# Performance work log

Hardware: AMD Instinct MI355X
Metric: run time of the kernel (lower is better)

Reference implementation:

```python
import jax, jax.numpy as jnp
import numpy as np
from jax import lax

B, S, D, STEPS, OUT = 512, 256, 256, 256, 3


def setup_inputs() -> dict:
    key = jax.random.key(0)
    ks = jax.random.split(key, 16)
    sc = 0.05
    n = lambda k, shp: jax.random.normal(k, shp, jnp.float32) * sc
    return {
        "e_all": jax.random.normal(ks[0], (B, S, D), jnp.float32),
        "e_last": jax.random.normal(ks[1], (1, B, D), jnp.float32),
        # NN_Attention params
        "Wa": n(ks[2], (D, D)), "ba": n(ks[3], (D,)),
        "Ua": n(ks[4], (D, D)), "bu": n(ks[5], (D,)),
        "Va": n(ks[6], (D,)), "bv": n(ks[7], ()),
        # GRU params (PyTorch layout: W_ih [3D, 3+D], W_hh [3D, D])
        "W_ih": n(ks[8], (3 * D, D + 3)), "b_ih": n(ks[9], (3 * D,)),
        "W_hh": n(ks[10], (3 * D, D)), "b_hh": n(ks[11], (3 * D,)),
        # output linear D -> 3
        "Wo": n(ks[12], (OUT, D)), "bo": n(ks[13], (OUT,)),
    }


def _decode(e_all, e_last, Wa, ba, Ua, bu, Va, bv, W_ih, b_ih, W_hh, b_hh, Wo, bo):
    # Ua(keys) is constant across steps -> precompute once (same math)
    Ua_keys = jnp.einsum('bsd,ed->bse', e_all, Ua) + bu  # [B, S, D]

    def step(carry, _):
        h, x_in = carry
        # Bahdanau attention: Va(tanh(Wa(q) + Ua(keys)))
        q = h @ Wa.T + ba                                       # [B, D]
        scores = jnp.einsum('bsd,d->bs', jnp.tanh(q[:, None, :] + Ua_keys), Va) + bv
        w = jax.nn.softmax(scores, axis=-1)                     # [B, S]
        ctx = jnp.einsum('bs,bsd->bd', w, e_all)                # [B, D]
        # GRU cell on input [context ; d_input] (cat order matches torch code)
        x = jnp.concatenate([ctx, x_in], axis=-1)               # [B, D+3]
        gi = x @ W_ih.T + b_ih
        gh = h @ W_hh.T + b_hh
        i_r, i_z, i_n = jnp.split(gi, 3, axis=-1)
        h_r, h_z, h_n = jnp.split(gh, 3, axis=-1)
        r = jax.nn.sigmoid(i_r + h_r)
        z = jax.nn.sigmoid(i_z + h_z)
        nn_ = jnp.tanh(i_n + r * h_n)
        h_new = (1.0 - z) * nn_ + z * h
        out = h_new @ Wo.T + bo                                 # [B, 3]
        return (h_new, out), (out, w)

    h0 = e_last[0]                                              # [B, D]
    x0 = jnp.zeros((h0.shape[0], OUT), h0.dtype)
    (hT, _), (outs, ws) = lax.scan(step, (h0, x0), None, length=STEPS)
    d_outputs = outs.transpose(1, 0, 2)                         # [B, STEPS, 3]
    cross_attn = ws.transpose(1, 0, 2).reshape(h0.shape[0], 1, STEPS * S)
    return d_outputs, hT[None], cross_attn


def reference(e_all, e_last, Wa, ba, Ua, bu, Va, bv, W_ih, b_ih, W_hh, b_hh, Wo, bo):
    return _decode(e_all, e_last, Wa, ba, Ua, bu, Va, bv, W_ih, b_ih, W_hh, b_hh, Wo, bo)
```

## Files before the change

### kernel.cpp

```cpp
#include <hip/hip_runtime.h>
#include <hip/hip_bf16.h>
#include <stdint.h>

#define NB 512
#define NS 256
#define ND 256
#define NT 256
#define NO 3

#define LOG2E 1.44269504088896340736f
#define C2 (2.0f*LOG2E)

#if __has_builtin(__builtin_amdgcn_exp2f)
__device__ __forceinline__ float exp2_fast(float x){ return __builtin_amdgcn_exp2f(x); }
#else
__device__ __forceinline__ float exp2_fast(float x){ return exp2f(x); }
#endif
#if __has_builtin(__builtin_amdgcn_rcpf)
__device__ __forceinline__ float rcp_fast(float x){ return __builtin_amdgcn_rcpf(x); }
#else
__device__ __forceinline__ float rcp_fast(float x){ return 1.0f/x; }
#endif

__device__ __forceinline__ float tanh_f(float x){
  float e = exp2_fast(x * C2);
  return 1.0f - 2.0f*rcp_fast(e + 1.0f);
}
__device__ __forceinline__ float sigm_f(float x){
  return rcp_fast(1.0f + exp2_fast(-x*LOG2E));
}
__device__ __forceinline__ float bflo(uint32_t u){ return __uint_as_float(u<<16); }
__device__ __forceinline__ float bfhi(uint32_t u){ return __uint_as_float(u & 0xffff0000u); }
__device__ __forceinline__ uint16_t f2bf(float f){
  uint32_t u = __float_as_uint(f);
  return (uint16_t)((u + 0x7fffu + ((u>>16)&1u)) >> 16);
}
__device__ __forceinline__ uint32_t pack2(float a, float b){
  return (uint32_t)f2bf(a) | ((uint32_t)f2bf(b) << 16);
}

#if __has_builtin(__builtin_amdgcn_fdot2_f32_bf16)
typedef __bf16 bfp2 __attribute__((ext_vector_type(2)));
__device__ __forceinline__ float dot2bf(uint32_t a, uint32_t b, float c){
  return __builtin_amdgcn_fdot2_f32_bf16(__builtin_bit_cast(bfp2, a),
                                         __builtin_bit_cast(bfp2, b), c, false);
}
#else
__device__ __forceinline__ float dot2bf(uint32_t a, uint32_t b, float c){
  return c + bflo(a)*bflo(b) + bfhi(a)*bfhi(b);
}
#endif


__global__ void k_transpose(const float* __restrict__ src, float* __restrict__ dst,
                            int R, int C){
  int idx = blockIdx.x*256 + threadIdx.x;
  if (idx < R*C){
    int r = idx / C, c = idx - r*C;
    dst[c*R + r] = src[idx];
  }
}

__global__ void __launch_bounds__(256) k_uk(const float* __restrict__ e_all,
    const float* __restrict__ UaT, const float* __restrict__ bu,
    uint16_t* __restrict__ UK){
  __shared__ float At[ND][20];
  const int t = threadIdx.x;
  const int m0 = blockIdx.x * 16;
  const int b  = m0 >> 8;
  const int s0 = m0 & (NS-1);
  #pragma unroll
  for (int i=0;i<16;i++)
    At[t][i] = e_all[(size_t)(m0+i)*ND + t];
  __syncthreads();
  float acc[16];
  float bue = bu[t];
  #pragma unroll
  for (int i=0;i<16;i++) acc[i] = bue;
  for (int d=0; d<ND; ++d){
    float u = UaT[d*ND + t];
    const float4 a0 = *(const float4*)&At[d][0];
    const float4 a1 = *(const float4*)&At[d][4];
    const float4 a2 = *(const float4*)&At[d][8];
    const float4 a3 = *(const float4*)&At[d][12];
    acc[0]+=a0.x*u;  acc[1]+=a0.y*u;  acc[2]+=a0.z*u;  acc[3]+=a0.w*u;
    acc[4]+=a1.x*u;  acc[5]+=a1.y*u;  acc[6]+=a1.z*u;  acc[7]+=a1.w*u;
    acc[8]+=a2.x*u;  acc[9]+=a2.y*u;  acc[10]+=a2.z*u; acc[11]+=a2.w*u;
    acc[12]+=a3.x*u; acc[13]+=a3.y*u; acc[14]+=a3.z*u; acc[15]+=a3.w*u;
  }
  const int e8 = t>>3, j = t&7;
  uint16_t* base = UK + (size_t)b*NS*ND + (size_t)e8*(NS*8) + j;
  #pragma unroll
  for (int i=0;i<16;i++)
    base[(size_t)(s0+i)*8] = f2bf(acc[i] * C2);
}

__global__ void k_ep(const float* __restrict__ e_all, uint32_t* __restrict__ EP){
  int idx = blockIdx.x*256 + threadIdx.x;
  if (idx >= NB*128*256) return;
  int d  = idx & 255;
  int s2 = (idx >> 8) & 127;
  int b  = idx >> 15;
  float e0 = e_all[((size_t)b*NS + 2*s2  )*ND + d];
  float e1 = e_all[((size_t)b*NS + 2*s2+1)*ND + d];
  EP[idx] = pack2(e0, e1);
}

__global__ void k_pkq(const float* __restrict__ W_ih, const float* __restrict__ W_hh,
                      uint32_t* __restrict__ PKq){
  int idx = blockIdx.x*256 + threadIdx.x;
  if (idx >= 260*3*256) return;
  int d  = idx & 255;
  int gk = idx >> 8;
  int k2 = gk/3, g = gk - 3*k2;
  int col = g*256 + d;
  float w0 = 0.f, w1 = 0.f;
  if (k2 < 130){
    int k0 = 2*k2, k1 = k0+1;
    w0 = W_ih[(size_t)col*259 + k0];
    w1 = (k1 < 259) ? W_ih[(size_t)col*259 + k1] : 0.f;
  } else if (k2 < 258){
    int kk = 2*(k2-130);
    w0 = W_hh[(size_t)col*256 + kk];
    w1 = W_hh[(size_t)col*256 + kk+1];
  }
  PKq[idx] = pack2(w0, w1);
}

__global__ void k_pack_q(const float* __restrict__ Wa, uint32_t* __restrict__ PQ){
  int idx = blockIdx.x*256 + threadIdx.x;
  if (idx >= 128*256) return;
  int d = idx & 255, k2 = idx >> 8;
  PQ[idx] = pack2(Wa[(size_t)d*256 + 2*k2], Wa[(size_t)d*256 + 2*k2 + 1]);
}

__global__ void __launch_bounds__(1024, 4) k_decode(
    const uint16_t* __restrict__ UK, const uint32_t* __restrict__ EP,
    const uint32_t* __restrict__ PKq, const uint32_t* __restrict__ PQ,
    const float* __restrict__ e_last,
    const float* __restrict__ Va, const float* __restrict__ bv,
    const float* __restrict__ b_ih, const float* __restrict__ b_hh,
    const float* __restrict__ ba, const float* __restrict__ bo,
    const float* __restrict__ Wo,
    float* __restrict__ dout, float* __restrict__ hT_out, float* __restrict__ ca)
{
  __shared__ float    hf[2][ND];
  __shared__ float    xin[2][4];
  __shared__ uint32_t xb[2][260];
  __shared__ __align__(16) float qL[2][ND];
  __shared__ __align__(16) float va2[ND];
  __shared__ float    WoL[3*ND];
  __shared__ float    qpart[2][2][ND];
  __shared__ float    spart[2][2][ND];
  __shared__ __align__(16) float cpart[2][8][ND];
  __shared__ float    gpart[2][4][3][ND];
  __shared__ uint32_t wb[2][128];
  __shared__ float    red[16];

  const int t    = threadIdx.x;
  const int d    = t & 255;
  const int q4   = t >> 8;
  const int bi   = q4 >> 1;
  const int half = q4 & 1;
  const int lane = t & 63;
  const int w    = t >> 6;
  const int b0   = blockIdx.x * 2;

  if (q4 == 0){
    hf[0][d] = e_last[(size_t)b0*ND + d];
    va2[d]   = 2.0f*Va[d];
    WoL[d] = Wo[d]; WoL[256+d] = Wo[256+d]; WoL[512+d] = Wo[512+d];
    if (d < 4){ xin[0][d]=0.f; xin[1][d]=0.f; }
  } else if (q4 == 1){
    hf[1][d] = e_last[(size_t)(b0+1)*ND + d];
  }
  const float bias_r  = b_ih[d]     + b_hh[d];
  const float bias_z  = b_ih[256+d] + b_hh[256+d];
  const float bias_ni = b_ih[512+d];
  const float bias_nh = b_hh[512+d];
  const float ba_d = ba[d];
  const float bv0  = bv[0];
  const float bo0 = bo[0], bo1 = bo[1], bo2 = bo[2];
  __syncthreads();
  if (t < 256){
    int bb = t>>7, i = t&127;
    xb[bb][130+i] = pack2(hf[bb][2*i], hf[bb][2*i+1]);
  }
  if (t == 256){
    xb[0][128]=0u; xb[0][129]=0u; xb[0][258]=0u; xb[0][259]=0u;
    xb[1][128]=0u; xb[1][129]=0u; xb[1][258]=0u; xb[1][259]=0u;
  }
  float sumVaH = 0.f;
  {
    #pragma unroll 8
    for (int e = half*128; e < half*128+128; ++e) sumVaH += va2[e];
    sumVaH *= 0.5f;
  }
  __syncthreads();

  const uint16_t* ukb  = UK + (size_t)(b0+bi)*NS*ND + (size_t)half*16*2048 + (size_t)d*8;
  const uint32_t* epbw = EP + (size_t)(b0+(w>>3))*128*256;
  float* ca_bq = ca + (size_t)(b0 + (q4&1))*(NT*NS);

  #pragma unroll 1
  for (int step=0; step<NT; ++step){
    {
      float aq = 0.f;
      const uint32_t* pq = PQ + (size_t)(half*64)*256 + d;
      const uint32_t* xh = &xb[bi][130 + half*64];
      #pragma unroll 1
      for (int kk=0; kk<64; kk+=8){
        uint32_t wv[8], xv[8];
        #pragma unroll
        for (int j=0;j<8;j++){ wv[j] = pq[(kk+j)*256]; xv[j] = xh[kk+j]; }
        #pragma unroll
        for (int j=0;j<8;j++) aq = dot2bf(wv[j], xv[j], aq);
      }
      qpart[bi][half][d] = aq;
    }
    __syncthreads();
    if (q4 < 2)
      qL[q4][d] = (qpart[q4][0][d] + qpart[q4][1][d] + ba_d) * C2;
    __syncthreads();

    {
      float acc = 0.f;
      #pragma unroll 1
      for (int g=0; g<16; g+=8){
        uint4 u[8];
        #pragma unroll
        for (int j=0;j<8;j++) u[j] = *(const uint4*)(ukb + (size_t)(g+j)*2048);
        #pragma unroll
        for (int j=0;j<8;j++){
          const int e0 = half*128 + (g+j)*8;
          const float4 q0 = *(const float4*)&qL[bi][e0];
          const float4 q1 = *(const float4*)&qL[bi][e0+4];
          const float4 v0 = *(const float4*)&va2[e0];
          const float4 v1 = *(const float4*)&va2[e0+4];
          float r;
          r = rcp_fast(exp2_fast(bflo(u[j].x)+q0.x)+1.f); acc = fmaf(v0.x, r, acc);
          r = rcp_fast(exp2_fast(bfhi(u[j].x)+q0.y)+1.f); acc = fmaf(v0.y, r, acc);
          r = rcp_fast(exp2_fast(bflo(u[j].y)+q0.z)+1.f); acc = fmaf(v0.z, r, acc);
          r = rcp_fast(exp2_fast(bfhi(u[j].y)+q0.w)+1.f); acc = fmaf(v0.w, r, acc);
          r = rcp_fast(exp2_fast(bflo(u[j].z)+q1.x)+1.f); acc = fmaf(v1.x, r, acc);
          r = rcp_fast(exp2_fast(bfhi(u[j].z)+q1.y)+1.f); acc = fmaf(v1.y, r, acc);
          r = rcp_fast(exp2_fast(bflo(u[j].w)+q1.z)+1.f); acc = fmaf(v1.z, r, acc);
          r = rcp_fast(exp2_fast(bfhi(u[j].w)+q1.w)+1.f); acc = fmaf(v1.w, r, acc);
        }
      }
      spart[bi][half][d] = sumVaH - acc;
    }
    __syncthreads();

    float p_reg = 0.f;
    if (q4 < 2){
      float sc = spart[q4][0][d] + spart[q4][1][d] + bv0;
      p_reg = exp2_fast(sc * LOG2E);
      float ssum = p_reg;
      #pragma unroll
      for (int o=32;o;o>>=1) ssum += __shfl_xor(ssum, o);
      if (lane==0) red[w] = ssum;
    }
    __syncthreads();
    if (q4 < 2){
      const int rb = q4*4;
      float ssum = (red[rb]+red[rb+1]) + (red[rb+2]+red[rb+3]);
      float wgt = p_reg * rcp_fast(ssum);
      __builtin_nontemporal_store(wgt, &ca_bq[(size_t)step*NS + d]);
      float other = __shfl_xor(wgt, 1);
      if (!(d&1)) wb[q4][d>>1] = pack2(wgt, other);
    }
    __syncthreads();

    {
      const int cb = w>>3, sub = w&7;
      float c0=0,c1=0,c2=0,c3=0;
      const int s0 = sub*16;
      #pragma unroll 1
      for (int g=0; g<16; g+=8){
        uint4 ev[8]; uint32_t wp[8];
        #pragma unroll
        for (int j=0;j<8;j++){
          ev[j] = *(const uint4*)(epbw + (size_t)(s0+g+j)*256 + lane*4);
          wp[j] = wb[cb][s0+g+j];
        }
        #pragma unroll
        for (int j=0;j<8;j++){
          c0 = dot2bf(ev[j].x, wp[j], c0);
          c1 = dot2bf(ev[j].y, wp[j], c1);
          c2 = dot2bf(ev[j].z, wp[j], c2);
          c3 = dot2bf(ev[j].w, wp[j], c3);
        }
      }
      *(float4*)&cpart[cb][sub][lane*4] = make_float4(c0,c1,c2,c3);
    }
    __syncthreads();
    if (q4 < 2){
      float cx = 0.f;
      #pragma unroll
      for (int i=0;i<8;i++) cx += cpart[q4][i][d];
      float other = __shfl_xor(cx, 1);
      if (!(d&1)) xb[q4][d>>1] = pack2(cx, other);
      if (d==128) xb[q4][128] = pack2(xin[q4][0], xin[q4][1]);
      if (d==129) xb[q4][129] = pack2(xin[q4][2], 0.f);
    }
    __syncthreads();

    {
      float a0r=0,a0z=0,a0n=0, a1r=0,a1z=0,a1n=0;
      const int k0 = q4*65;
      const uint32_t* pk = PKq + (size_t)k0*768 + d;
      #pragma unroll 1
      for (int g=0; g<64; g+=8){
        uint32_t wr[8], wz[8], wn[8], x0[8], x1[8];
        #pragma unroll
        for (int j=0;j<8;j++){
          const uint32_t* p = pk + (size_t)(g+j)*768;
          wr[j]=p[0]; wz[j]=p[256]; wn[j]=p[512];
          x0[j]=xb[0][k0+g+j]; x1[j]=xb[1][k0+g+j];
        }
        #pragma unroll
        for (int j=0;j<8;j++){
          a0r=dot2bf(wr[j],x0[j],a0r); a0z=dot2bf(wz[j],x0[j],a0z); a0n=dot2bf(wn[j],x0[j],a0n);
          a1r=dot2bf(wr[j],x1[j],a1r); a1z=dot2bf(wz[j],x1[j],a1z); a1n=dot2bf(wn[j],x1[j],a1n);
        }
      }
      {
        const uint32_t* p = pk + (size_t)64*768;
        uint32_t w0=p[0], w1=p[256], w2=p[512];
        uint32_t xa=xb[0][k0+64], xc=xb[1][k0+64];
        a0r=dot2bf(w0,xa,a0r); a0z=dot2bf(w1,xa,a0z); a0n=dot2bf(w2,xa,a0n);
        a1r=dot2bf(w0,xc,a1r); a1z=dot2bf(w1,xc,a1z); a1n=dot2bf(w2,xc,a1n);
      }
      gpart[0][q4][0][d]=a0r; gpart[0][q4][1][d]=a0z; gpart[0][q4][2][d]=a0n;
      gpart[1][q4][0][d]=a1r; gpart[1][q4][1][d]=a1z; gpart[1][q4][2][d]=a1n;
    }
    __syncthreads();
    if (q4 < 2){
      float ar  = (gpart[q4][0][0][d]+gpart[q4][1][0][d]) + (gpart[q4][2][0][d]+gpart[q4][3][0][d]) + bias_r;
      float az  = (gpart[q4][0][1][d]+gpart[q4][1][1][d]) + (gpart[q4][2][1][d]+gpart[q4][3][1][d]) + bias_z;
      float ani =  gpart[q4][0][2][d]+gpart[q4][1][2][d] + bias_ni;
      float anh =  gpart[q4][2][2][d]+gpart[q4][3][2][d] + bias_nh;
      float rg = sigm_f(ar);
      float zg = sigm_f(az);
      float ng = tanh_f(ani + rg*anh);
      float hnew = (1.f-zg)*ng + zg*hf[q4][d];
      hf[q4][d] = hnew;
      float other = __shfl_xor(hnew, 1);
      if (!(d&1)) xb[q4][130 + (d>>1)] = pack2(hnew, other);
    }
    __syncthreads();

    if ((w & 7) == 0){
      const int bq = w >> 3;
      float p0=0,p1=0,p2=0;
      #pragma unroll
      for (int i=0;i<4;i++){
        float hv = hf[bq][i*64 + lane];
        p0 = fmaf(hv, WoL[      i*64+lane], p0);
        p1 = fmaf(hv, WoL[256 + i*64+lane], p1);
        p2 = fmaf(hv, WoL[512 + i*64+lane], p2);
      }
      #pragma unroll
      for (int o=32;o;o>>=1){
        p0+=__shfl_xor(p0,o); p1+=__shfl_xor(p1,o); p2+=__shfl_xor(p2,o);
      }
      if (lane==0){
        float o0=p0+bo0, o1=p1+bo1, o2=p2+bo2;
        float* do_b = dout + (size_t)(b0+bq)*(NT*NO);
        __builtin_nontemporal_store(o0, &do_b[(size_t)step*NO+0]);
        __builtin_nontemporal_store(o1, &do_b[(size_t)step*NO+1]);
        __builtin_nontemporal_store(o2, &do_b[(size_t)step*NO+2]);
        xin[bq][0]=o0; xin[bq][1]=o1; xin[bq][2]=o2;
      }
    }
  }

  __syncthreads();
  if (q4 < 2) hT_out[(size_t)(b0+q4)*ND + d] = hf[q4][d];
}


extern "C" void kernel_launch(void* const* d_in, const int* in_sizes, int n_in,
                              void* d_out, int out_size, void* d_ws, size_t ws_size,
                              hipStream_t stream) {
  const float* e_all  = (const float*)d_in[0];
  const float* e_last = (const float*)d_in[1];
  const float* Wa     = (const float*)d_in[2];
  const float* ba     = (const float*)d_in[3];
  const float* Ua     = (const float*)d_in[4];
  const float* bu     = (const float*)d_in[5];
  const float* Va     = (const float*)d_in[6];
  const float* bv     = (const float*)d_in[7];
  const float* W_ih   = (const float*)d_in[8];
  const float* b_ih   = (const float*)d_in[9];
  const float* W_hh   = (const float*)d_in[10];
  const float* b_hh   = (const float*)d_in[11];
  const float* Wo     = (const float*)d_in[12];
  const float* bo     = (const float*)d_in[13];

  char* ws = (char*)d_ws;
  uint16_t* UK   = (uint16_t*)(ws + 0ull);
  uint32_t* EP   = (uint32_t*)(ws + 67108864ull);
  float*    UaT  = (float*)(ws + 134217728ull);
  uint32_t* PKq  = (uint32_t*)(ws + 134217728ull);
  uint32_t* PQ   = (uint32_t*)(ws + 135016448ull);

  float* dout = (float*)d_out;
  float* hT   = dout + (size_t)NB*NT*NO;
  float* ca   = hT   + (size_t)NB*ND;

  k_transpose<<<(ND*ND+255)/256,256,0,stream>>>(Ua, UaT, ND, ND);
  k_uk<<<NB*NS/16,256,0,stream>>>(e_all, UaT, bu, UK);
  k_ep<<<(NB*128*256+255)/256,256,0,stream>>>(e_all, EP);
  k_pkq<<<(260*3*256+255)/256,256,0,stream>>>(W_ih, W_hh, PKq);
  k_pack_q<<<(128*256+255)/256,256,0,stream>>>(Wa, PQ);

  k_decode<<<NB/2,1024,0,stream>>>(UK, EP, PKq, PQ, e_last, Va, bv,
                                   b_ih, b_hh, ba, bo, Wo, dout, hT, ca);
}
```

Baseline: 7.738 ms.

## Use MFMA bf16 for query projection and GRU gate matmuls per step

Replaces the per-step dot2 bf16 loops for the Wa query projection and the GRU input/hidden gate products with 16x16x32 bf16 MFMA instructions. A 16-row LDS panel holds the two batch rows (context, previous output, hidden) padded to 16, and each wave computes 16 output columns. Weights are repacked row-major in bf16 for MFMA B operands, and the partial-sum LDS buffers and their extra syncs are removed. The cost is that 14 of the 16 MFMA rows are wasted padding, and B operands are read from global memory each step.

Measured after the change: 15.08 ms. 1.95x slower.

```diff
diff --git a/kernel.cpp b/kernel.cpp
--- a/kernel.cpp
+++ b/kernel.cpp
@@ -7,9 +7,14 @@
 #define ND 256
 #define NT 256
 #define NO 3
+#define KG 544
+#define PROW 552
 
 #define LOG2E 1.44269504088896340736f
 #define C2 (2.0f*LOG2E)
+
+typedef short short8v __attribute__((ext_vector_type(8)));
+typedef float f32x4   __attribute__((ext_vector_type(4)));
 
 #if __has_builtin(__builtin_amdgcn_exp2f)
 __device__ __forceinline__ float exp2_fast(float x){ return __builtin_amdgcn_exp2f(x); }
@@ -50,6 +55,10 @@
   return c + bflo(a)*bflo(b) + bfhi(a)*bfhi(b);
 }
 #endif
+
+__device__ __forceinline__ f32x4 mfma_bf16(short8v a, short8v b, f32x4 c){
+  return __builtin_amdgcn_mfma_f32_16x16x32_bf16(a, b, c, 0, 0, 0);
+}
 
 
 __global__ void k_transpose(const float* __restrict__ src, float* __restrict__ dst,
@@ -106,37 +115,26 @@
   EP[idx] = pack2(e0, e1);
 }
 
-__global__ void k_pkq(const float* __restrict__ W_ih, const float* __restrict__ W_hh,
-                      uint32_t* __restrict__ PKq){
+__global__ void k_wg(const float* __restrict__ W_ih, const float* __restrict__ W_hh,
+                     uint16_t* __restrict__ Wg){
   int idx = blockIdx.x*256 + threadIdx.x;
-  if (idx >= 260*3*256) return;
-  int d  = idx & 255;
-  int gk = idx >> 8;
-  int k2 = gk/3, g = gk - 3*k2;
-  int col = g*256 + d;
-  float w0 = 0.f, w1 = 0.f;
-  if (k2 < 130){
-    int k0 = 2*k2, k1 = k0+1;
-    w0 = W_ih[(size_t)col*259 + k0];
-    w1 = (k1 < 259) ? W_ih[(size_t)col*259 + k1] : 0.f;
-  } else if (k2 < 258){
-    int kk = 2*(k2-130);
-    w0 = W_hh[(size_t)col*256 + kk];
-    w1 = W_hh[(size_t)col*256 + kk+1];
-  }
-  PKq[idx] = pack2(w0, w1);
-}
-
-__global__ void k_pack_q(const float* __restrict__ Wa, uint32_t* __restrict__ PQ){
+  if (idx >= 768*KG) return;
+  int n = idx / KG, k = idx - n*KG;
+  float v = 0.f;
+  if (k < 259)       v = W_ih[(size_t)n*259 + k];
+  else if (k >= 288) v = W_hh[(size_t)n*256 + (k-288)];
+  Wg[idx] = f2bf(v);
+}
+
+__global__ void k_wq(const float* __restrict__ Wa, uint16_t* __restrict__ Wq){
   int idx = blockIdx.x*256 + threadIdx.x;
-  if (idx >= 128*256) return;
-  int d = idx & 255, k2 = idx >> 8;
-  PQ[idx] = pack2(Wa[(size_t)d*256 + 2*k2], Wa[(size_t)d*256 + 2*k2 + 1]);
+  if (idx >= ND*ND) return;
+  Wq[idx] = f2bf(Wa[idx]);
 }
 
 __global__ void __launch_bounds__(1024, 4) k_decode(
     const uint16_t* __restrict__ UK, const uint32_t* __restrict__ EP,
-    const uint32_t* __restrict__ PKq, const uint32_t* __restrict__ PQ,
+    const uint16_t* __restrict__ Wg, const uint16_t* __restrict__ Wq,
     const float* __restrict__ e_last,
     const float* __restrict__ Va, const float* __restrict__ bv,
     const float* __restrict__ b_ih, const float* __restrict__ b_hh,
@@ -144,16 +142,14 @@
     const float* __restrict__ Wo,
     float* __restrict__ dout, float* __restrict__ hT_out, float* __restrict__ ca)
 {
+  __shared__ __align__(16) uint16_t panelA[16*PROW];
   __shared__ float    hf[2][ND];
   __shared__ float    xin[2][4];
-  __shared__ uint32_t xb[2][260];
   __shared__ __align__(16) float qL[2][ND];
   __shared__ __align__(16) float va2[ND];
   __shared__ float    WoL[3*ND];
-  __shared__ float    qpart[2][2][ND];
   __shared__ float    spart[2][2][ND];
   __shared__ __align__(16) float cpart[2][8][ND];
-  __shared__ float    gpart[2][4][3][ND];
   __shared__ uint32_t wb[2][128];
   __shared__ float    red[16];
 
@@ -166,30 +162,23 @@
   const int w    = t >> 6;
   const int b0   = blockIdx.x * 2;
 
+  for (int i=t; i<16*PROW; i+=1024) panelA[i] = 0;
   if (q4 == 0){
-    hf[0][d] = e_last[(size_t)b0*ND + d];
-    va2[d]   = 2.0f*Va[d];
+    va2[d] = 2.0f*Va[d];
     WoL[d] = Wo[d]; WoL[256+d] = Wo[256+d]; WoL[512+d] = Wo[512+d];
     if (d < 4){ xin[0][d]=0.f; xin[1][d]=0.f; }
-  } else if (q4 == 1){
-    hf[1][d] = e_last[(size_t)(b0+1)*ND + d];
-  }
-  const float bias_r  = b_ih[d]     + b_hh[d];
-  const float bias_z  = b_ih[256+d] + b_hh[256+d];
-  const float bias_ni = b_ih[512+d];
-  const float bias_nh = b_hh[512+d];
-  const float ba_d = ba[d];
-  const float bv0  = bv[0];
+  }
+  if (q4 < 2) hf[q4][d] = e_last[(size_t)(b0+q4)*ND + d];
+  const int ncol = (w<<4) + (lane & 15);
+  const float biasR  = b_ih[ncol]     + b_hh[ncol];
+  const float biasZ  = b_ih[256+ncol] + b_hh[256+ncol];
+  const float biasNi = b_ih[512+ncol];
+  const float biasNh = b_hh[512+ncol];
+  const float baq    = ba[ncol];
+  const float bv0 = bv[0];
   const float bo0 = bo[0], bo1 = bo[1], bo2 = bo[2];
   __syncthreads();
-  if (t < 256){
-    int bb = t>>7, i = t&127;
-    xb[bb][130+i] = pack2(hf[bb][2*i], hf[bb][2*i+1]);
-  }
-  if (t == 256){
-    xb[0][128]=0u; xb[0][129]=0u; xb[0][258]=0u; xb[0][259]=0u;
-    xb[1][128]=0u; xb[1][129]=0u; xb[1][258]=0u; xb[1][259]=0u;
-  }
+  if (q4 < 2) panelA[q4*PROW + 288 + d] = f2bf(hf[q4][d]);
   float sumVaH = 0.f;
   {
     #pragma unroll 8
@@ -202,25 +191,28 @@
   const uint32_t* epbw = EP + (size_t)(b0+(w>>3))*128*256;
   float* ca_bq = ca + (size_t)(b0 + (q4&1))*(NT*NS);
 
+  const uint16_t* apG = panelA + (lane&15)*PROW + ((lane>>4)*8);
+  const uint16_t* apQ = apG + 288;
+  const uint16_t* bQ  = Wq + (size_t)(ncol)*ND + ((lane>>4)*8);
+  const uint16_t* bR  = Wg + (size_t)(ncol)*KG + ((lane>>4)*8);
+  const uint16_t* bZ  = bR + (size_t)256*KG;
+  const uint16_t* bN  = bR + (size_t)512*KG;
+
   #pragma unroll 1
   for (int step=0; step<NT; ++step){
     {
-      float aq = 0.f;
-      const uint32_t* pq = PQ + (size_t)(half*64)*256 + d;
-      const uint32_t* xh = &xb[bi][130 + half*64];
-      #pragma unroll 1
-      for (int kk=0; kk<64; kk+=8){
-        uint32_t wv[8], xv[8];
-        #pragma unroll
-        for (int j=0;j<8;j++){ wv[j] = pq[(kk+j)*256]; xv[j] = xh[kk+j]; }
-        #pragma unroll
-        for (int j=0;j<8;j++) aq = dot2bf(wv[j], xv[j], aq);
-      }
-      qpart[bi][half][d] = aq;
-    }
-    __syncthreads();
-    if (q4 < 2)
-      qL[q4][d] = (qpart[q4][0][d] + qpart[q4][1][d] + ba_d) * C2;
+      f32x4 aq = {0.f,0.f,0.f,0.f};
+      #pragma unroll
+      for (int ks=0; ks<8; ++ks){
+        short8v av = *(const short8v*)(apQ + ks*32);
+        short8v bvv= *(const short8v*)(bQ  + ks*32);
+        aq = mfma_bf16(av, bvv, aq);
+      }
+      if (lane < 16){
+        qL[0][ncol] = (aq[0] + baq) * C2;
+        qL[1][ncol] = (aq[1] + baq) * C2;
+      }
+    }
     __syncthreads();
 
     {
@@ -299,55 +291,40 @@
       float cx = 0.f;
       #pragma unroll
       for (int i=0;i<8;i++) cx += cpart[q4][i][d];
-      float other = __shfl_xor(cx, 1);
-      if (!(d&1)) xb[q4][d>>1] = pack2(cx, other);
-      if (d==128) xb[q4][128] = pack2(xin[q4][0], xin[q4][1]);
-      if (d==129) xb[q4][129] = pack2(xin[q4][2], 0.f);
+      panelA[q4*PROW + d] = f2bf(cx);
+      if (d < 3) panelA[q4*PROW + 256 + d] = f2bf(xin[q4][d]);
     }
     __syncthreads();
 
     {
-      float a0r=0,a0z=0,a0n=0, a1r=0,a1z=0,a1n=0;
-      const int k0 = q4*65;
-      const uint32_t* pk = PKq + (size_t)k0*768 + d;
-      #pragma unroll 1
-      for (int g=0; g<64; g+=8){
-        uint32_t wr[8], wz[8], wn[8], x0[8], x1[8];
-        #pragma unroll
-        for (int j=0;j<8;j++){
-          const uint32_t* p = pk + (size_t)(g+j)*768;
-          wr[j]=p[0]; wz[j]=p[256]; wn[j]=p[512];
-          x0[j]=xb[0][k0+g+j]; x1[j]=xb[1][k0+g+j];
+      f32x4 aR = {0,0,0,0}, aZ = {0,0,0,0}, aNi = {0,0,0,0}, aNh = {0,0,0,0};
+      #pragma unroll
+      for (int ks=0; ks<9; ++ks){
+        short8v av = *(const short8v*)(apG + ks*32);
+        aR  = mfma_bf16(av, *(const short8v*)(bR + ks*32), aR);
+        aZ  = mfma_bf16(av, *(const short8v*)(bZ + ks*32), aZ);
+        aNi = mfma_bf16(av, *(const short8v*)(bN + ks*32), aNi);
+      }
+      #pragma unroll
+      for (int ks=9; ks<17; ++ks){
+        short8v av = *(const short8v*)(apG + ks*32);
+        aR  = mfma_bf16(av, *(const short8v*)(bR + ks*32), aR);
+        aZ  = mfma_bf16(av, *(const short8v*)(bZ + ks*32), aZ);
+        aNh = mfma_bf16(av, *(const short8v*)(bN + ks*32), aNh);
+      }
+      __syncthreads();
+      if (lane < 16){
+        #pragma unroll
+        for (int m=0; m<2; ++m){
+          float rg = sigm_f(aR[m] + biasR);
+          float zg = sigm_f(aZ[m] + biasZ);
+          float ng = tanh_f((aNi[m] + biasNi) + rg*(aNh[m] + biasNh));
+          float hold = hf[m][ncol];
+          float hnew = (1.f - zg)*ng + zg*hold;
+          hf[m][ncol] = hnew;
+          panelA[m*PROW + 288 + ncol] = f2bf(hnew);
         }
-        #pragma unroll
-        for (int j=0;j<8;j++){
-          a0r=dot2bf(wr[j],x0[j],a0r); a0z=dot2bf(wz[j],x0[j],a0z); a0n=dot2bf(wn[j],x0[j],a0n);
-          a1r=dot2bf(wr[j],x1[j],a1r); a1z=dot2bf(wz[j],x1[j],a1z); a1n=dot2bf(wn[j],x1[j],a1n);
-        }
-      }
-      {
-        const uint32_t* p = pk + (size_t)64*768;
-        uint32_t w0=p[0], w1=p[256], w2=p[512];
-        uint32_t xa=xb[0][k0+64], xc=xb[1][k0+64];
-        a0r=dot2bf(w0,xa,a0r); a0z=dot2bf(w1,xa,a0z); a0n=dot2bf(w2,xa,a0n);
-        a1r=dot2bf(w0,xc,a1r); a1z=dot2bf(w1,xc,a1z); a1n=dot2bf(w2,xc,a1n);
-      }
-      gpart[0][q4][0][d]=a0r; gpart[0][q4][1][d]=a0z; gpart[0][q4][2][d]=a0n;
-      gpart[1][q4][0][d]=a1r; gpart[1][q4][1][d]=a1z; gpart[1][q4][2][d]=a1n;
-    }
-    __syncthreads();
-    if (q4 < 2){
-      float ar  = (gpart[q4][0][0][d]+gpart[q4][1][0][d]) + (gpart[q4][2][0][d]+gpart[q4][3][0][d]) + bias_r;
-      float az  = (gpart[q4][0][1][d]+gpart[q4][1][1][d]) + (gpart[q4][2][1][d]+gpart[q4][3][1][d]) + bias_z;
-      float ani =  gpart[q4][0][2][d]+gpart[q4][1][2][d] + bias_ni;
-      float anh =  gpart[q4][2][2][d]+gpart[q4][3][2][d] + bias_nh;
-      float rg = sigm_f(ar);
-      float zg = sigm_f(az);
-      float ng = tanh_f(ani + rg*anh);
-      float hnew = (1.f-zg)*ng + zg*hf[q4][d];
-      hf[q4][d] = hnew;
-      float other = __shfl_xor(hnew, 1);
-      if (!(d&1)) xb[q4][130 + (d>>1)] = pack2(hnew, other);
+      }
     }
     __syncthreads();
 
@@ -400,11 +377,11 @@
   const float* bo     = (const float*)d_in[13];
 
   char* ws = (char*)d_ws;
-  uint16_t* UK   = (uint16_t*)(ws + 0ull);
-  uint32_t* EP   = (uint32_t*)(ws + 67108864ull);
-  float*    UaT  = (float*)(ws + 134217728ull);
-  uint32_t* PKq  = (uint32_t*)(ws + 134217728ull);
-  uint32_t* PQ   = (uint32_t*)(ws + 135016448ull);
+  uint16_t* UK  = (uint16_t*)(ws + 0ull);
+  uint32_t* EP  = (uint32_t*)(ws + 67108864ull);
+  uint16_t* Wg  = (uint16_t*)(ws + 134217728ull);
+  uint16_t* Wq  = (uint16_t*)(ws + 135053312ull);
+  float*    UaT = (float*)   (ws + 135184384ull);
 
   float* dout = (float*)d_out;
   float* hT   = dout + (size_t)NB*NT*NO;
@@ -413,9 +390,9 @@
   k_transpose<<<(ND*ND+255)/256,256,0,stream>>>(Ua, UaT, ND, ND);
   k_uk<<<NB*NS/16,256,0,stream>>>(e_all, UaT, bu, UK);
   k_ep<<<(NB*128*256+255)/256,256,0,stream>>>(e_all, EP);
-  k_pkq<<<(260*3*256+255)/256,256,0,stream>>>(W_ih, W_hh, PKq);
-  k_pack_q<<<(128*256+255)/256,256,0,stream>>>(Wa, PQ);
-
-  k_decode<<<NB/2,1024,0,stream>>>(UK, EP, PKq, PQ, e_last, Va, bv,
+  k_wg<<<(768*KG+255)/256,256,0,stream>>>(W_ih, W_hh, Wg);
+  k_wq<<<(ND*ND+255)/256,256,0,stream>>>(Wa, Wq);
+
+  k_decode<<<NB/2,1024,0,stream>>>(UK, EP, Wg, Wq, e_last, Va, bv,
                                    b_ih, b_hh, ba, bo, Wo, dout, hT, ca);
 }
```

## Store precomputed keys and encoder states as FP8 E4M3 instead of bf16

Applied to the files above, without the earlier changes.

The precomputed Ua(keys) tensor and the packed encoder states are now quantized to FP8 E4M3, with custom encode kernels, new interleaved layouts and hardware fp8-to-f32 packed conversion in the decode loop. This halves the bytes the per-step attention and context loops stream from global memory or cache on every decode step. The cost is much coarser precision on activations (3-bit mantissa), which may exceed the accuracy tolerance, plus added conversion instructions in the hot loops.

After: 16.39 ms. 2.12x slower.

```diff
diff --git a/kernel.cpp b/kernel.cpp
--- a/kernel.cpp
+++ b/kernel.cpp
@@ -10,6 +10,8 @@
 
 #define LOG2E 1.44269504088896340736f
 #define C2 (2.0f*LOG2E)
+
+typedef float f32x2 __attribute__((ext_vector_type(2)));
 
 #if __has_builtin(__builtin_amdgcn_exp2f)
 __device__ __forceinline__ float exp2_fast(float x){ return __builtin_amdgcn_exp2f(x); }
@@ -51,6 +53,47 @@
 }
 #endif
 
+__device__ __forceinline__ uint8_t enc_e4m3(float x){
+  uint32_t sign = (__float_as_uint(x) >> 31) << 7;
+  float y = fminf(fabsf(x), 448.0f);
+  uint32_t u = __float_as_uint(y);
+  int e = (int)(u >> 23) - 127;
+  uint32_t code;
+  if (e < -6){
+    code = (uint32_t)__float2int_rn(y * 512.0f);
+  } else {
+    uint32_t r = u + 0x000FFFFFu + ((u >> 20) & 1u);
+    e = (int)(r >> 23) - 127;
+    code = (uint32_t)((e + 7) << 3) | ((r >> 20) & 7u);
+    if (code > 0x7Eu) code = 0x7Eu;
+  }
+  return (uint8_t)(sign | code);
+}
+
+#if __has_builtin(__builtin_amdgcn_cvt_pk_f32_fp8)
+template<bool HI>
+__device__ __forceinline__ f32x2 cvtpk_fp8(uint32_t w){
+  return __builtin_amdgcn_cvt_pk_f32_fp8((int)w, HI);
+}
+#else
+__device__ __forceinline__ float dec1_e4m3(uint32_t b){
+  uint32_t s = (b >> 7) << 31;
+  uint32_t em = b & 0x7fu;
+  float mag;
+  if (em >= 8u){
+    mag = __uint_as_float((((em >> 3) + 120u) << 23) | ((em & 7u) << 20));
+  } else {
+    mag = (float)em * 0.001953125f;
+  }
+  return __uint_as_float(s | __float_as_uint(mag));
+}
+template<bool HI>
+__device__ __forceinline__ f32x2 cvtpk_fp8(uint32_t w){
+  uint32_t p = HI ? (w >> 16) : (w & 0xffffu);
+  f32x2 r; r.x = dec1_e4m3(p & 0xffu); r.y = dec1_e4m3(p >> 8); return r;
+}
+#endif
+
 
 __global__ void k_transpose(const float* __restrict__ src, float* __restrict__ dst,
                             int R, int C){
@@ -63,7 +106,7 @@
 
 __global__ void __launch_bounds__(256) k_uk(const float* __restrict__ e_all,
     const float* __restrict__ UaT, const float* __restrict__ bu,
-    uint16_t* __restrict__ UK){
+    uint8_t* __restrict__ UKQ){
   __shared__ float At[ND][20];
   const int t = threadIdx.x;
   const int m0 = blockIdx.x * 16;
@@ -88,22 +131,29 @@
     acc[8]+=a2.x*u;  acc[9]+=a2.y*u;  acc[10]+=a2.z*u; acc[11]+=a2.w*u;
     acc[12]+=a3.x*u; acc[13]+=a3.y*u; acc[14]+=a3.z*u; acc[15]+=a3.w*u;
   }
-  const int e8 = t>>3, j = t&7;
-  uint16_t* base = UK + (size_t)b*NS*ND + (size_t)e8*(NS*8) + j;
+  const int e16 = t>>4, j = t&15;
+  uint8_t* base = UKQ + (((size_t)b*16 + e16)*256 + s0)*16 + j;
   #pragma unroll
-  for (int i=0;i<16;i++)
-    base[(size_t)(s0+i)*8] = f2bf(acc[i] * C2);
-}
-
-__global__ void k_ep(const float* __restrict__ e_all, uint32_t* __restrict__ EP){
+  for (int i=0;i<16;i++){
+    uint32_t mine = enc_e4m3(acc[i] * C2);
+    uint32_t other = (uint32_t)__shfl_xor((int)mine, 1);
+    if (!(t & 1))
+      *(uint16_t*)(base + (size_t)i*16) = (uint16_t)(mine | (other << 8));
+  }
+}
+
+__global__ void k_epq(const float* __restrict__ e_all, uint32_t* __restrict__ EPQ){
   int idx = blockIdx.x*256 + threadIdx.x;
-  if (idx >= NB*128*256) return;
+  if (idx >= NB*64*256) return;
   int d  = idx & 255;
-  int s2 = (idx >> 8) & 127;
-  int b  = idx >> 15;
-  float e0 = e_all[((size_t)b*NS + 2*s2  )*ND + d];
-  float e1 = e_all[((size_t)b*NS + 2*s2+1)*ND + d];
-  EP[idx] = pack2(e0, e1);
+  int s4 = (idx >> 8) & 63;
+  int b  = idx >> 14;
+  const float* e = e_all + ((size_t)b*NS + 4*s4)*ND + d;
+  uint32_t v = (uint32_t)enc_e4m3(e[0])
+             | ((uint32_t)enc_e4m3(e[ND])   << 8)
+             | ((uint32_t)enc_e4m3(e[2*ND]) << 16)
+             | ((uint32_t)enc_e4m3(e[3*ND]) << 24);
+  EPQ[idx] = v;
 }
 
 __global__ void k_pkq(const float* __restrict__ W_ih, const float* __restrict__ W_hh,
@@ -135,7 +185,7 @@
 }
 
 __global__ void __launch_bounds__(1024, 4) k_decode(
-    const uint16_t* __restrict__ UK, const uint32_t* __restrict__ EP,
+    const uint8_t* __restrict__ UKQ, const uint32_t* __restrict__ EPQ,
     const uint32_t* __restrict__ PKq, const uint32_t* __restrict__ PQ,
     const float* __restrict__ e_last,
     const float* __restrict__ Va, const float* __restrict__ bv,
@@ -154,7 +204,7 @@
   __shared__ float    spart[2][2][ND];
   __shared__ __align__(16) float cpart[2][8][ND];
   __shared__ float    gpart[2][4][3][ND];
-  __shared__ uint32_t wb[2][128];
+  __shared__ __align__(16) float wl[2][NS];
   __shared__ float    red[16];
 
   const int t    = threadIdx.x;
@@ -198,8 +248,8 @@
   }
   __syncthreads();
 
-  const uint16_t* ukb  = UK + (size_t)(b0+bi)*NS*ND + (size_t)half*16*2048 + (size_t)d*8;
-  const uint32_t* epbw = EP + (size_t)(b0+(w>>3))*128*256;
+  const uint8_t*  ukq  = UKQ + (((size_t)(b0+bi)*16 + half*8)*256 + d)*16;
+  const uint32_t* epqw = EPQ + (size_t)(b0+(w>>3))*64*256;
   float* ca_bq = ca + (size_t)(b0 + (q4&1))*(NT*NS);
 
   #pragma unroll 1
@@ -225,27 +275,25 @@
 
     {
       float acc = 0.f;
-      #pragma unroll 1
-      for (int g=0; g<16; g+=8){
-        uint4 u[8];
+      uint4 u[8];
+      #pragma unroll
+      for (int j=0;j<8;j++) u[j] = *(const uint4*)(ukq + (size_t)j*4096);
+      #pragma unroll
+      for (int j=0;j<8;j++){
+        const int e0g = half*128 + j*16;
         #pragma unroll
-        for (int j=0;j<8;j++) u[j] = *(const uint4*)(ukb + (size_t)(g+j)*2048);
-        #pragma unroll
-        for (int j=0;j<8;j++){
-          const int e0 = half*128 + (g+j)*8;
-          const float4 q0 = *(const float4*)&qL[bi][e0];
-          const float4 q1 = *(const float4*)&qL[bi][e0+4];
-          const float4 v0 = *(const float4*)&va2[e0];
-          const float4 v1 = *(const float4*)&va2[e0+4];
+        for (int dw=0; dw<4; ++dw){
+          const uint32_t dwv = (dw==0)?u[j].x:(dw==1)?u[j].y:(dw==2)?u[j].z:u[j].w;
+          const int eb = e0g + dw*4;
+          const f32x2 lo = cvtpk_fp8<false>(dwv);
+          const f32x2 hi = cvtpk_fp8<true>(dwv);
+          const float4 qq = *(const float4*)&qL[bi][eb];
+          const float4 vv = *(const float4*)&va2[eb];
           float r;
-          r = rcp_fast(exp2_fast(bflo(u[j].x)+q0.x)+1.f); acc = fmaf(v0.x, r, acc);
-          r = rcp_fast(exp2_fast(bfhi(u[j].x)+q0.y)+1.f); acc = fmaf(v0.y, r, acc);
-          r = rcp_fast(exp2_fast(bflo(u[j].y)+q0.z)+1.f); acc = fmaf(v0.z, r, acc);
-          r = rcp_fast(exp2_fast(bfhi(u[j].y)+q0.w)+1.f); acc = fmaf(v0.w, r, acc);
-          r = rcp_fast(exp2_fast(bflo(u[j].z)+q1.x)+1.f); acc = fmaf(v1.x, r, acc);
-          r = rcp_fast(exp2_fast(bfhi(u[j].z)+q1.y)+1.f); acc = fmaf(v1.y, r, acc);
-          r = rcp_fast(exp2_fast(bflo(u[j].w)+q1.z)+1.f); acc = fmaf(v1.z, r, acc);
-          r = rcp_fast(exp2_fast(bfhi(u[j].w)+q1.w)+1.f); acc = fmaf(v1.w, r, acc);
+          r = rcp_fast(exp2_fast(lo.x + qq.x) + 1.f); acc = fmaf(vv.x, r, acc);
+          r = rcp_fast(exp2_fast(lo.y + qq.y) + 1.f); acc = fmaf(vv.y, r, acc);
+          r = rcp_fast(exp2_fast(hi.x + qq.z) + 1.f); acc = fmaf(vv.z, r, acc);
+          r = rcp_fast(exp2_fast(hi.y + qq.w) + 1.f); acc = fmaf(vv.w, r, acc);
         }
       }
       spart[bi][half][d] = sumVaH - acc;
@@ -267,30 +315,29 @@
       float ssum = (red[rb]+red[rb+1]) + (red[rb+2]+red[rb+3]);
       float wgt = p_reg * rcp_fast(ssum);
       __builtin_nontemporal_store(wgt, &ca_bq[(size_t)step*NS + d]);
-      float other = __shfl_xor(wgt, 1);
-      if (!(d&1)) wb[q4][d>>1] = pack2(wgt, other);
+      wl[q4][d] = wgt;
     }
     __syncthreads();
 
     {
       const int cb = w>>3, sub = w&7;
       float c0=0,c1=0,c2=0,c3=0;
-      const int s0 = sub*16;
-      #pragma unroll 1
-      for (int g=0; g<16; g+=8){
-        uint4 ev[8]; uint32_t wp[8];
-        #pragma unroll
-        for (int j=0;j<8;j++){
-          ev[j] = *(const uint4*)(epbw + (size_t)(s0+g+j)*256 + lane*4);
-          wp[j] = wb[cb][s0+g+j];
-        }
-        #pragma unroll
-        for (int j=0;j<8;j++){
-          c0 = dot2bf(ev[j].x, wp[j], c0);
-          c1 = dot2bf(ev[j].y, wp[j], c1);
-          c2 = dot2bf(ev[j].z, wp[j], c2);
-          c3 = dot2bf(ev[j].w, wp[j], c3);
-        }
+      uint4 ev[8];
+      #pragma unroll
+      for (int i=0;i<8;i++)
+        ev[i] = *(const uint4*)(epqw + (size_t)(sub*8+i)*256 + lane*4);
+      #pragma unroll
+      for (int i=0;i<8;i++){
+        const float4 w4 = *(const float4*)&wl[cb][(sub*8+i)*4];
+        f32x2 lo, hi;
+        lo = cvtpk_fp8<false>(ev[i].x); hi = cvtpk_fp8<true>(ev[i].x);
+        c0 = fmaf(w4.x,lo.x, fmaf(w4.y,lo.y, fmaf(w4.z,hi.x, fmaf(w4.w,hi.y, c0))));
+        lo = cvtpk_fp8<false>(ev[i].y); hi = cvtpk_fp8<true>(ev[i].y);
+        c1 = fmaf(w4.x,lo.x, fmaf(w4.y,lo.y, fmaf(w4.z,hi.x, fmaf(w4.w,hi.y, c1))));
+        lo = cvtpk_fp8<false>(ev[i].z); hi = cvtpk_fp8<true>(ev[i].z);
+        c2 = fmaf(w4.x,lo.x, fmaf(w4.y,lo.y, fmaf(w4.z,hi.x, fmaf(w4.w,hi.y, c2))));
+        lo = cvtpk_fp8<false>(ev[i].w); hi = cvtpk_fp8<true>(ev[i].w);
+        c3 = fmaf(w4.x,lo.x, fmaf(w4.y,lo.y, fmaf(w4.z,hi.x, fmaf(w4.w,hi.y, c3))));
       }
       *(float4*)&cpart[cb][sub][lane*4] = make_float4(c0,c1,c2,c3);
     }
@@ -400,22 +447,22 @@
   const float* bo     = (const float*)d_in[13];
 
   char* ws = (char*)d_ws;
-  uint16_t* UK   = (uint16_t*)(ws + 0ull);
-  uint32_t* EP   = (uint32_t*)(ws + 67108864ull);
-  float*    UaT  = (float*)(ws + 134217728ull);
-  uint32_t* PKq  = (uint32_t*)(ws + 134217728ull);
-  uint32_t* PQ   = (uint32_t*)(ws + 135016448ull);
+  uint8_t*  UKQ = (uint8_t*) (ws + 0ull);
+  uint32_t* EPQ = (uint32_t*)(ws + 33554432ull);
+  uint32_t* PKq = (uint32_t*)(ws + 67108864ull);
+  uint32_t* PQ  = (uint32_t*)(ws + 67907584ull);
+  float*    UaT = (float*)   (ws + 68038656ull);
 
   float* dout = (float*)d_out;
   float* hT   = dout + (size_t)NB*NT*NO;
   float* ca   = hT   + (size_t)NB*ND;
 
   k_transpose<<<(ND*ND+255)/256,256,0,stream>>>(Ua, UaT, ND, ND);
-  k_uk<<<NB*NS/16,256,0,stream>>>(e_all, UaT, bu, UK);
-  k_ep<<<(NB*128*256+255)/256,256,0,stream>>>(e_all, EP);
+  k_uk<<<NB*NS/16,256,0,stream>>>(e_all, UaT, bu, UKQ);
+  k_epq<<<(NB*64*256+255)/256,256,0,stream>>>(e_all, EPQ);
   k_pkq<<<(260*3*256+255)/256,256,0,stream>>>(W_ih, W_hh, PKq);
   k_pack_q<<<(128*256+255)/256,256,0,stream>>>(Wa, PQ);
 
-  k_decode<<<NB/2,1024,0,stream>>>(UK, EP, PKq, PQ, e_last, Va, bv,
+  k_decode<<<NB/2,1024,0,stream>>>(UKQ, EPQ, PKq, PQ, e_last, Va, bv,
                                    b_ih, b_hh, ba, bo, Wo, dout, hT, ca);
 }
```
